# Kernel tuning notes

Hardware: AMD Instinct MI355X
Metric: run time of the kernel (lower is better)

The kernel has to match this reference:

```python
import jax, jax.numpy as jnp
import numpy as np

N_NODES = 30000
N_EDGES = 960000
HIDDEN = 256
HEADS = 4
S = 15  # num_samples
K_DIFF = 4
ALPHA = 0.1
BETA = 0.9
EPS_BN = 1e-5


def _mlp(x, W, b, g, bt, a):
    # Linear -> BatchNorm (eval: running_mean=0, running_var=1) -> PReLU
    h = x @ W + b
    h = g * h / jnp.sqrt(jnp.asarray(1.0 + EPS_BN, h.dtype)) + bt
    return jnp.where(h >= 0, h, a * h)


def _mgdcf(x, src, dst, n, k, alpha, beta):
    # Markov graph diffusion: h_k = alpha*x + beta * A_hat h_{k-1}, A_hat = D^-1/2 A D^-1/2
    ones = jnp.ones(src.shape[0], dtype=x.dtype)
    deg = jnp.maximum(jax.ops.segment_sum(ones, dst, num_segments=n), 1.0)
    norm = jax.lax.rsqrt(deg[src] * deg[dst])  # [E]
    h = x
    for _ in range(k):
        msg = jax.ops.segment_sum(h[src] * norm[:, None], dst, num_segments=n)
        h = alpha * x + beta * msg
    z = alpha * (1.0 - beta ** k) / (1.0 - beta) + beta ** k  # scale normalizer
    return h / z


def _mha(mem, Wq, bq, Wk, bk, Wv, bv, Wo, bo):
    # small-window multi-head self-attention with residual, no LN/FF
    n, s, hdim = mem.shape
    hd = hdim // HEADS
    q = (mem @ Wq + bq).reshape(n, s, HEADS, hd)
    k = (mem @ Wk + bk).reshape(n, s, HEADS, hd)
    v = (mem @ Wv + bv).reshape(n, s, HEADS, hd)
    scores = jnp.einsum('nqhd,nkhd->nhqk', q, k) / np.float32(np.sqrt(hd))
    attn = jax.nn.softmax(scores, axis=-1)
    out = jnp.einsum('nhqk,nkhd->nqhd', attn, v).reshape(n, s, hdim)
    return out @ Wo + bo + mem


def setup_inputs() -> dict:
    key = jax.random.key(0)
    ks = jax.random.split(key, 16)
    d = {}
    d['text_feat'] = jax.random.normal(ks[0], (N_NODES, 768), jnp.float32)
    d['visual_feat'] = jax.random.normal(ks[1], (N_NODES, 512), jnp.float32)
    d['edge_index'] = jax.random.randint(ks[2], (2, N_EDGES), 0, N_NODES, jnp.int32)
    d['memory_index'] = jax.random.randint(ks[3], (N_NODES, S), 0, N_NODES, jnp.int32)
    d['t_W'] = jax.random.normal(ks[4], (768, HIDDEN), jnp.float32) * np.float32(768 ** -0.5)
    d['t_b'] = jnp.zeros((HIDDEN,), jnp.float32)
    d['t_gamma'] = jnp.ones((HIDDEN,), jnp.float32)
    d['t_beta'] = jnp.zeros((HIDDEN,), jnp.float32)
    d['t_a'] = jnp.asarray(0.25, jnp.float32)
    d['v_W'] = jax.random.normal(ks[5], (512, HIDDEN), jnp.float32) * np.float32(512 ** -0.5)
    d['v_b'] = jnp.zeros((HIDDEN,), jnp.float32)
    d['v_gamma'] = jnp.ones((HIDDEN,), jnp.float32)
    d['v_beta'] = jnp.zeros((HIDDEN,), jnp.float32)
    d['v_a'] = jnp.asarray(0.25, jnp.float32)
    sc = np.float32(HIDDEN ** -0.5)
    d['Wq'] = jax.random.normal(ks[6], (HIDDEN, HIDDEN), jnp.float32) * sc
    d['bq'] = jnp.zeros((HIDDEN,), jnp.float32)
    d['Wk'] = jax.random.normal(ks[7], (HIDDEN, HIDDEN), jnp.float32) * sc
    d['bk'] = jnp.zeros((HIDDEN,), jnp.float32)
    d['Wv'] = jax.random.normal(ks[8], (HIDDEN, HIDDEN), jnp.float32) * sc
    d['bv'] = jnp.zeros((HIDDEN,), jnp.float32)
    d['Wo'] = jax.random.normal(ks[9], (HIDDEN, HIDDEN), jnp.float32) * sc
    d['bo'] = jnp.zeros((HIDDEN,), jnp.float32)
    d['Wc'] = jax.random.normal(ks[10], (HIDDEN, 40), jnp.float32) * sc
    d['bc'] = jnp.zeros((40,), jnp.float32)
    return d


def reference(text_feat, visual_feat, edge_index, memory_index,
              t_W, t_b, t_gamma, t_beta, t_a,
              v_W, v_b, v_gamma, v_beta, v_a,
              Wq, bq, Wk, bk, Wv, bv, Wo, bo, Wc, bc):
    n = text_feat.shape[0]
    src, dst = edge_index[0], edge_index[1]
    enc_t = _mlp(text_feat, t_W, t_b, t_gamma, t_beta, t_a)
    enc_v = _mlp(visual_feat, v_W, v_b, v_gamma, v_beta, v_a)
    t_h = _mgdcf(enc_t, src, dst, n, K_DIFF, ALPHA, BETA)
    v_h = _mgdcf(enc_v, src, dst, n, K_DIFF, ALPHA, BETA)
    combined = t_h + v_h  # [N, H]
    # random-memory gather: [N, S+1, H]
    mem = jnp.concatenate([combined[:, None, :], combined[memory_index]], axis=1)
    z_memory_h = _mha(mem, Wq, bq, Wk, bk, Wv, bv, Wo, bo)
    final_h = z_memory_h[:, 0]
    logits = final_h @ Wc + bc
    return logits, final_h, z_memory_h
```

## Files before the change

kernel.cpp:

```cpp
#include <hip/hip_runtime.h>
#include <math.h>

#define NN 30000
#define NE 960000
#define HID 256
#define NH 4
#define HD 64

typedef __attribute__((ext_vector_type(8))) __bf16 bf16x8;
typedef __attribute__((ext_vector_type(4))) float f32x4;
typedef __attribute__((ext_vector_type(4))) unsigned int u32x4;
typedef __attribute__((ext_vector_type(4))) unsigned short u16x4;

__device__ __forceinline__ unsigned short f2bf(float f) {
    unsigned u = __builtin_bit_cast(unsigned, f);
    u += 0x7fffu + ((u >> 16) & 1u);
    return (unsigned short)(u >> 16);
}
__device__ __forceinline__ float bf2f(unsigned short h) {
    unsigned u = ((unsigned)h) << 16;
    return __builtin_bit_cast(float, u);
}

__global__ void wsplit_k(const float* __restrict__ W, int K, int N,
                         unsigned short* __restrict__ Wh,
                         unsigned short* __restrict__ Wl)
{
    const int gid = blockIdx.x * 256 + threadIdx.x;
    if (gid >= K * N) return;
    const int k = gid / N, n = gid - k * N;
    const float f = W[gid];
    const unsigned short h = f2bf(f);
    const float lo = f - bf2f(h);
    Wh[(size_t)n * K + k] = h;
    Wl[(size_t)n * K + k] = f2bf(lo);
}

#define TBM 128
#define TBN 128
#define TBK 32
#define LDK 40

__global__ void __launch_bounds__(256) gemm_mfma(
    const float* __restrict__ A,
    const unsigned short* __restrict__ Wth,
    const unsigned short* __restrict__ Wtl,
    const float* __restrict__ bias,
    const float* __restrict__ gamma, const float* __restrict__ beta2,
    const float* __restrict__ a_ptr,
    float* __restrict__ C, int M, int N, int K, int mode)
{
    __shared__ unsigned short Ah[TBM * LDK];
    __shared__ unsigned short Al[TBM * LDK];
    __shared__ unsigned short Bh[TBN * LDK];
    __shared__ unsigned short Bl[TBN * LDK];

    const int t = threadIdx.x;
    const int bm = blockIdx.y * TBM;
    const int bn = blockIdx.x * TBN;
    const int wid = t >> 6, lane = t & 63;
    const int wm = (wid >> 1) * 64;
    const int wn = (wid & 1) * 64;
    const int fr = lane & 15;
    const int kg = lane >> 4;

    const int arow = t >> 3;
    const int ak   = (t & 7) * 4;

    f32x4 acc[4][4] = {};

    for (int k0 = 0; k0 < K; k0 += TBK) {
#pragma unroll
        for (int r = 0; r < 4; r++) {
            const int row = r * 32 + arow;
            const int gr = bm + row;
            float4 av = make_float4(0.f, 0.f, 0.f, 0.f);
            if (gr < M) av = *(const float4*)(A + (size_t)gr * K + k0 + ak);
            const unsigned short h0 = f2bf(av.x), h1 = f2bf(av.y),
                                 h2 = f2bf(av.z), h3 = f2bf(av.w);
            const unsigned short l0 = f2bf(av.x - bf2f(h0)),
                                 l1 = f2bf(av.y - bf2f(h1)),
                                 l2 = f2bf(av.z - bf2f(h2)),
                                 l3 = f2bf(av.w - bf2f(h3));
            u16x4 hv; hv.x = h0; hv.y = h1; hv.z = h2; hv.w = h3;
            u16x4 lv; lv.x = l0; lv.y = l1; lv.z = l2; lv.w = l3;
            *(u16x4*)&Ah[row * LDK + ak] = hv;
            *(u16x4*)&Al[row * LDK + ak] = lv;
        }
#pragma unroll
        for (int i2 = 0; i2 < 2; i2++) {
            const int i = i2 * 256 + t;
            const int n = i >> 2, kc = (i & 3) * 8;
            const size_t g = (size_t)(bn + n) * K + k0 + kc;
            *(u32x4*)&Bh[n * LDK + kc] = *(const u32x4*)&Wth[g];
            *(u32x4*)&Bl[n * LDK + kc] = *(const u32x4*)&Wtl[g];
        }
        __syncthreads();

        bf16x8 fah[4], fal[4], fbh[4], fbl[4];
#pragma unroll
        for (int mf = 0; mf < 4; mf++) {
            const int off = (wm + mf * 16 + fr) * LDK + kg * 8;
            fah[mf] = *(const bf16x8*)&Ah[off];
            fal[mf] = *(const bf16x8*)&Al[off];
        }
#pragma unroll
        for (int nf = 0; nf < 4; nf++) {
            const int off = (wn + nf * 16 + fr) * LDK + kg * 8;
            fbh[nf] = *(const bf16x8*)&Bh[off];
            fbl[nf] = *(const bf16x8*)&Bl[off];
        }
#pragma unroll
        for (int mf = 0; mf < 4; mf++) {
#pragma unroll
            for (int nf = 0; nf < 4; nf++) {
                acc[mf][nf] = __builtin_amdgcn_mfma_f32_16x16x32_bf16(
                    fah[mf], fbh[nf], acc[mf][nf], 0, 0, 0);
                acc[mf][nf] = __builtin_amdgcn_mfma_f32_16x16x32_bf16(
                    fah[mf], fbl[nf], acc[mf][nf], 0, 0, 0);
                acc[mf][nf] = __builtin_amdgcn_mfma_f32_16x16x32_bf16(
                    fal[mf], fbh[nf], acc[mf][nf], 0, 0, 0);
            }
        }
        __syncthreads();
    }

    const float invs = 1.0f / sqrtf(1.0f + 1e-5f);
    const float av_ = (mode != 0) ? *a_ptr : 0.f;
#pragma unroll
    for (int nf = 0; nf < 4; nf++) {
        const int c = bn + wn + nf * 16 + fr;
        const float bi = bias[c];
        float gm = 0.f, bt = 0.f;
        if (mode != 0) { gm = gamma[c]; bt = beta2[c]; }
#pragma unroll
        for (int mf = 0; mf < 4; mf++) {
#pragma unroll
            for (int i = 0; i < 4; i++) {
                const int r = bm + wm + mf * 16 + kg * 4 + i;
                if (r < M) {
                    float h = acc[mf][nf][i] + bi;
                    if (mode != 0) {
                        h = gm * h * invs + bt;
                        h = (h >= 0.f) ? h : av_ * h;
                    }
                    float* cp = C + (size_t)r * N + c;
                    if (mode == 2) h += *cp;
                    *cp = h;
                }
            }
        }
    }
}

__global__ void count_k(const int* __restrict__ dst, int* __restrict__ counts)
{
    const int e = blockIdx.x * 256 + threadIdx.x;
    if (e < NE) atomicAdd(&counts[dst[e]], 1);
}

__global__ void deg_k(const int* __restrict__ counts, float* __restrict__ deg)
{
    const int i = blockIdx.x * 256 + threadIdx.x;
    if (i < NN) deg[i] = fmaxf((float)counts[i], 1.0f);
}

__global__ void __launch_bounds__(1024) scan_k(const int* __restrict__ counts,
                                               int* __restrict__ offs, int n)
{
    __shared__ int buf[1024];
    __shared__ int carry;
    const int t = threadIdx.x;
    if (t == 0) { carry = 0; offs[0] = 0; }
    __syncthreads();
    for (int base = 0; base < n; base += 1024) {
        const int i = base + t;
        int v = (i < n) ? counts[i] : 0;
        buf[t] = v;
        __syncthreads();
        for (int off = 1; off < 1024; off <<= 1) {
            int add = (t >= off) ? buf[t - off] : 0;
            __syncthreads();
            buf[t] += add;
            __syncthreads();
        }
        if (i < n) offs[i + 1] = carry + buf[t];
        __syncthreads();
        if (t == 0) carry += buf[1023];
        __syncthreads();
    }
}

__global__ void fill_k(const int* __restrict__ src, const int* __restrict__ dst,
                       const int* __restrict__ offs, int* __restrict__ cursor,
                       const float* __restrict__ deg,
                       int* __restrict__ csrc, float* __restrict__ cw)
{
    const int e = blockIdx.x * 256 + threadIdx.x;
    if (e < NE) {
        const int d = dst[e];
        const int s = src[e];
        const int p = atomicAdd(&cursor[d], 1);
        const int slot = offs[d] + p;
        csrc[slot] = s;
        cw[slot] = rsqrtf(deg[s] * deg[d]);
    }
}

__global__ void __launch_bounds__(256) spmv_k(
    const float* __restrict__ hin, const float* __restrict__ x,
    const int* __restrict__ offs, const int* __restrict__ csrc,
    const float* __restrict__ cw, float* __restrict__ hout, float scale)
{
    const int node = blockIdx.x;
    const int t = threadIdx.x;
    const int g = t >> 6;
    const int lane = t & 63;
    const int start = offs[node], end = offs[node + 1];
    __shared__ int   ss[256];
    __shared__ float sw[256];
    __shared__ float part[4][256];
    float4 acc = make_float4(0.f, 0.f, 0.f, 0.f);
    for (int base = start; base < end; base += 256) {
        const int cnt = min(256, end - base);
        __syncthreads();
        if (t < cnt) { ss[t] = csrc[base + t]; sw[t] = cw[base + t]; }
        __syncthreads();
        for (int j = g; j < cnt; j += 4) {
            const float w = sw[j];
            const float4 v = *(const float4*)(hin + (size_t)ss[j] * HID + lane * 4);
            acc.x += v.x * w; acc.y += v.y * w;
            acc.z += v.z * w; acc.w += v.w * w;
        }
    }
    *(float4*)&part[g][lane * 4] = acc;
    __syncthreads();
    const float s = part[0][t] + part[1][t] + part[2][t] + part[3][t];
    const size_t o = (size_t)node * HID + t;
    hout[o] = (0.1f * x[o] + 0.9f * s) * scale;
}

__global__ void build_wvo(const float* __restrict__ Wv, const float* __restrict__ Wo,
                          const float* __restrict__ bv,
                          float* __restrict__ Wvo, float* __restrict__ bvo)
{
    const int gid = blockIdx.x * 256 + threadIdx.x;
    if (gid < 256 * 1024) {
        const int k = gid >> 10;
        const int col = gid & 1023;
        const int h = col >> 8, j = col & 255;
        float s = 0.f;
#pragma unroll 8
        for (int d = 0; d < HD; d++)
            s += Wv[k * HID + h * HD + d] * Wo[(h * HD + d) * HID + j];
        Wvo[(size_t)k * 1024 + col] = s;
    } else if (gid < 256 * 1024 + 1024) {
        const int col = gid - 256 * 1024;
        const int h = col >> 8, j = col & 255;
        float s = 0.f;
#pragma unroll 8
        for (int d = 0; d < HD; d++)
            s += bv[h * HD + d] * Wo[(h * HD + d) * HID + j];
        bvo[col] = s;
    }
}

__global__ void __launch_bounds__(256) attn_k(
    const float* __restrict__ Cq, const float* __restrict__ Ck,
    const float* __restrict__ P, const float* __restrict__ comb,
    const int* __restrict__ midx, const float* __restrict__ bo,
    const float* __restrict__ Wc, const float* __restrict__ bc,
    float* __restrict__ zout, float* __restrict__ fhout, float* __restrict__ lout)
{
    __shared__ float qs[16][260];
    __shared__ float ks[16][260];
    __shared__ float at2[16][NH][16];
    __shared__ float row0[256];
    __shared__ int   idx[16];
    const int n = blockIdx.x;
    const int t = threadIdx.x;

    if (t < 16) idx[t] = (t == 0) ? n : midx[n * 15 + t - 1];
    __syncthreads();
    int idr[16];
#pragma unroll
    for (int r = 0; r < 16; r++) idr[r] = idx[r];
#pragma unroll
    for (int r = 0; r < 16; r++) {
        const size_t g = (size_t)idr[r] * HID + t;
        qs[r][t] = Cq[g];
        ks[r][t] = Ck[g];
    }

    float pv[16][4];
#pragma unroll
    for (int k2 = 0; k2 < 16; k2++) {
        const float* pb = P + (size_t)idr[k2] * 1024 + t;
        pv[k2][0] = pb[0];
        pv[k2][1] = pb[256];
        pv[k2][2] = pb[512];
        pv[k2][3] = pb[768];
    }
    float cmb[16];
#pragma unroll
    for (int q2 = 0; q2 < 16; q2++)
        cmb[q2] = comb[(size_t)idr[q2] * HID + t];
    const float bov = bo[t];

    __syncthreads();

    const int kr = t & 15, qr = t >> 4;
#pragma unroll
    for (int h = 0; h < NH; h++) {
        float s = 0.f;
#pragma unroll
        for (int i = 0; i < HD; i++)
            s += qs[qr][h * HD + i] * ks[kr][h * HD + i];
        s *= 0.125f;
        float m = s;
        m = fmaxf(m, __shfl_xor(m, 1));
        m = fmaxf(m, __shfl_xor(m, 2));
        m = fmaxf(m, __shfl_xor(m, 4));
        m = fmaxf(m, __shfl_xor(m, 8));
        const float e = __expf(s - m);
        float sum = e;
        sum += __shfl_xor(sum, 1);
        sum += __shfl_xor(sum, 2);
        sum += __shfl_xor(sum, 4);
        sum += __shfl_xor(sum, 8);
        at2[qr][h][kr] = e / sum;
    }
    __syncthreads();

    float acc[16];
#pragma unroll
    for (int q2 = 0; q2 < 16; q2++) acc[q2] = cmb[q2] + bov;

#pragma unroll
    for (int q2 = 0; q2 < 16; q2++) {
        float s = acc[q2];
#pragma unroll
        for (int h = 0; h < NH; h++) {
            const f32x4* ap = (const f32x4*)&at2[q2][h][0];
            const f32x4 a0 = ap[0], a1 = ap[1], a2 = ap[2], a3 = ap[3];
            s += a0.x * pv[0][h]  + a0.y * pv[1][h]  + a0.z * pv[2][h]  + a0.w * pv[3][h]
               + a1.x * pv[4][h]  + a1.y * pv[5][h]  + a1.z * pv[6][h]  + a1.w * pv[7][h]
               + a2.x * pv[8][h]  + a2.y * pv[9][h]  + a2.z * pv[10][h] + a2.w * pv[11][h]
               + a3.x * pv[12][h] + a3.y * pv[13][h] + a3.z * pv[14][h] + a3.w * pv[15][h];
        }
        acc[q2] = s;
    }

#pragma unroll
    for (int q2 = 0; q2 < 16; q2++)
        zout[((size_t)n * 16 + q2) * HID + t] = acc[q2];
    row0[t] = acc[0];
    fhout[(size_t)n * HID + t] = acc[0];
    __syncthreads();
    if (t < 40) {
        float s = bc[t];
#pragma unroll 8
        for (int c = 0; c < 256; c++) s += row0[c] * Wc[c * 40 + t];
        lout[(size_t)n * 40 + t] = s;
    }
}

extern "C" void kernel_launch(void* const* d_in, const int* in_sizes, int n_in,
                              void* d_out, int out_size, void* d_ws, size_t ws_size,
                              hipStream_t stream)
{
    const float* text = (const float*)d_in[0];
    const float* vis  = (const float*)d_in[1];
    const int*   eidx = (const int*)d_in[2];
    const int*   midx = (const int*)d_in[3];
    const float* tW = (const float*)d_in[4];
    const float* tb = (const float*)d_in[5];
    const float* tg = (const float*)d_in[6];
    const float* tbe = (const float*)d_in[7];
    const float* ta = (const float*)d_in[8];
    const float* vW = (const float*)d_in[9];
    const float* vb = (const float*)d_in[10];
    const float* vg = (const float*)d_in[11];
    const float* vbe = (const float*)d_in[12];
    const float* va = (const float*)d_in[13];
    const float* Wq = (const float*)d_in[14];
    const float* bq = (const float*)d_in[15];
    const float* Wk = (const float*)d_in[16];
    const float* bk = (const float*)d_in[17];
    const float* Wv = (const float*)d_in[18];
    const float* bv = (const float*)d_in[19];
    const float* Wo = (const float*)d_in[20];
    const float* bo = (const float*)d_in[21];
    const float* Wc = (const float*)d_in[22];
    const float* bc = (const float*)d_in[23];

    float* out_logits = (float*)d_out;
    float* out_fh = out_logits + (size_t)NN * 40;
    float* out_z  = out_fh + (size_t)NN * HID;

    const size_t SLOT = (size_t)NN * HID;
    float* s_x   = (float*)d_ws;
    float* s_h1  = s_x + SLOT;
    float* s_h2  = s_h1 + SLOT;
    float* s_cq  = s_h2 + SLOT;
    float* s_ck  = s_cq + SLOT;
    float* s_P   = s_ck + SLOT;
    float* s_wvo = s_P + (size_t)NN * 1024;
    float* s_bvo = s_wvo + 256 * 1024;
    float* c_deg = s_bvo + 1024;
    int* c_counts = (int*)(c_deg + NN);
    int* c_off    = c_counts + NN;
    int* c_cursor = c_off + (NN + 1);
    int* c_src    = c_cursor + NN;
    float* c_w    = (float*)(c_src + NE);

    const int* e_src = eidx;
    const int* e_dst = eidx + NE;

    hipMemsetAsync(c_counts, 0, NN * sizeof(int), stream);
    hipMemsetAsync(c_cursor, 0, NN * sizeof(int), stream);

    unsigned short* tWh = (unsigned short*)s_h1;
    unsigned short* tWl = tWh + 768 * 256;
    unsigned short* vWh = tWl + 768 * 256;
    unsigned short* vWl = vWh + 512 * 256;
    wsplit_k<<<768, 256, 0, stream>>>(tW, 768, 256, tWh, tWl);
    wsplit_k<<<512, 256, 0, stream>>>(vW, 512, 256, vWh, vWl);

    const dim3 gE(HID / TBN, (NN + TBM - 1) / TBM);

    gemm_mfma<<<gE, 256, 0, stream>>>(text, tWh, tWl, tb, tg, tbe, ta, s_x, NN, HID, 768, 1);
    gemm_mfma<<<gE, 256, 0, stream>>>(vis,  vWh, vWl, vb, vg, vbe, va, s_x, NN, HID, 512, 2);

    count_k<<<NE / 256, 256, 0, stream>>>(e_dst, c_counts);
    deg_k<<<(NN + 255) / 256, 256, 0, stream>>>(c_counts, c_deg);
    scan_k<<<1, 1024, 0, stream>>>(c_counts, c_off, NN);
    fill_k<<<NE / 256, 256, 0, stream>>>(e_src, e_dst, c_off, c_cursor, c_deg, c_src, c_w);

    const double beta_k = 0.9 * 0.9 * 0.9 * 0.9;
    const double zd = 0.1 * (1.0 - beta_k) / (1.0 - 0.9) + beta_k;
    const float invz = (float)(1.0 / zd);
    spmv_k<<<NN, 256, 0, stream>>>(s_x,  s_x, c_off, c_src, c_w, s_h1, 1.0f);
    spmv_k<<<NN, 256, 0, stream>>>(s_h1, s_x, c_off, c_src, c_w, s_h2, 1.0f);
    spmv_k<<<NN, 256, 0, stream>>>(s_h2, s_x, c_off, c_src, c_w, s_h1, 1.0f);
    spmv_k<<<NN, 256, 0, stream>>>(s_h1, s_x, c_off, c_src, c_w, s_h2, invz);

    unsigned short* qWh = (unsigned short*)s_h1;
    unsigned short* qWl = qWh + 256 * 256;
    unsigned short* kWh = qWl + 256 * 256;
    unsigned short* kWl = kWh + 256 * 256;
    unsigned short* pWh = kWl + 256 * 256;
    unsigned short* pWl = pWh + 256 * 1024;
    wsplit_k<<<256, 256, 0, stream>>>(Wq, 256, 256, qWh, qWl);
    wsplit_k<<<256, 256, 0, stream>>>(Wk, 256, 256, kWh, kWl);
    build_wvo<<<(256 * 1024 + 1024) / 256, 256, 0, stream>>>(Wv, Wo, bv, s_wvo, s_bvo);
    wsplit_k<<<1024, 256, 0, stream>>>(s_wvo, 256, 1024, pWh, pWl);

    gemm_mfma<<<gE, 256, 0, stream>>>(s_h2, qWh, qWl, bq, nullptr, nullptr, nullptr, s_cq, NN, HID, HID, 0);
    gemm_mfma<<<gE, 256, 0, stream>>>(s_h2, kWh, kWl, bk, nullptr, nullptr, nullptr, s_ck, NN, HID, HID, 0);
    const dim3 gP(1024 / TBN, (NN + TBM - 1) / TBM);
    gemm_mfma<<<gP, 256, 0, stream>>>(s_h2, pWh, pWl, s_bvo, nullptr, nullptr, nullptr, s_P, NN, 1024, HID, 0);

    attn_k<<<NN, 256, 0, stream>>>(s_cq, s_ck, s_P, s_h2, midx, bo, Wc, bc,
                                   out_z, out_fh, out_logits);
}
```

Baseline: 2.275 ms.

## Compute attention scores with split-bf16 MFMA and stream z_memory stores

The scalar 64-wide dot products for the 16x16 per-head attention scores are replaced by MFMA 16x16x32 bf16 instructions, one wave per head. Q and K are stored in shared memory as high and low bf16 halves, and three MFMAs (hh, hl, lh) give close to fp32 accuracy. The change also adds a launch_bounds occupancy hint of 2 and writes the large zout tensor with nontemporal stores to avoid cache pollution. The costs are extra conversion ALU work and a small loss of precision compared with full fp32.

```diff
diff --git a/kernel.cpp b/kernel.cpp
--- a/kernel.cpp
+++ b/kernel.cpp
@@ -265,15 +265,17 @@
     }
 }
 
-__global__ void __launch_bounds__(256) attn_k(
+__global__ void __launch_bounds__(256, 2) attn_k(
     const float* __restrict__ Cq, const float* __restrict__ Ck,
     const float* __restrict__ P, const float* __restrict__ comb,
     const int* __restrict__ midx, const float* __restrict__ bo,
     const float* __restrict__ Wc, const float* __restrict__ bc,
     float* __restrict__ zout, float* __restrict__ fhout, float* __restrict__ lout)
 {
-    __shared__ float qs[16][260];
-    __shared__ float ks[16][260];
+    __shared__ unsigned short Qh[16][264];
+    __shared__ unsigned short Ql[16][264];
+    __shared__ unsigned short Kh[16][264];
+    __shared__ unsigned short Kl[16][264];
     __shared__ float at2[16][NH][16];
     __shared__ float row0[256];
     __shared__ int   idx[16];
@@ -285,12 +287,6 @@
     int idr[16];
 #pragma unroll
     for (int r = 0; r < 16; r++) idr[r] = idx[r];
-#pragma unroll
-    for (int r = 0; r < 16; r++) {
-        const size_t g = (size_t)idr[r] * HID + t;
-        qs[r][t] = Cq[g];
-        ks[r][t] = Ck[g];
-    }
 
     float pv[16][4];
 #pragma unroll
@@ -307,28 +303,50 @@
         cmb[q2] = comb[(size_t)idr[q2] * HID + t];
     const float bov = bo[t];
 
-    __syncthreads();
-
-    const int kr = t & 15, qr = t >> 4;
-#pragma unroll
-    for (int h = 0; h < NH; h++) {
-        float s = 0.f;
-#pragma unroll
-        for (int i = 0; i < HD; i++)
-            s += qs[qr][h * HD + i] * ks[kr][h * HD + i];
-        s *= 0.125f;
+#pragma unroll
+    for (int r = 0; r < 16; r++) {
+        const size_t g = (size_t)idr[r] * HID + t;
+        const float q = Cq[g];
+        const float k = Ck[g];
+        const unsigned short qh = f2bf(q);
+        const unsigned short kh = f2bf(k);
+        Qh[r][t] = qh; Ql[r][t] = f2bf(q - bf2f(qh));
+        Kh[r][t] = kh; Kl[r][t] = f2bf(k - bf2f(kh));
+    }
+    __syncthreads();
+
+    const int w  = t >> 6;
+    const int lw = t & 63;
+    const int fr = lw & 15;
+    const int kg = lw >> 4;
+
+    f32x4 sc = {};
+#pragma unroll
+    for (int ks = 0; ks < 2; ks++) {
+        const int off = w * 64 + ks * 32 + kg * 8;
+        const bf16x8 fqh = *(const bf16x8*)&Qh[fr][off];
+        const bf16x8 fql = *(const bf16x8*)&Ql[fr][off];
+        const bf16x8 fkh = *(const bf16x8*)&Kh[fr][off];
+        const bf16x8 fkl = *(const bf16x8*)&Kl[fr][off];
+        sc = __builtin_amdgcn_mfma_f32_16x16x32_bf16(fqh, fkh, sc, 0, 0, 0);
+        sc = __builtin_amdgcn_mfma_f32_16x16x32_bf16(fqh, fkl, sc, 0, 0, 0);
+        sc = __builtin_amdgcn_mfma_f32_16x16x32_bf16(fql, fkh, sc, 0, 0, 0);
+    }
+#pragma unroll
+    for (int i = 0; i < 4; i++) {
+        const float s = sc[i] * 0.125f;
         float m = s;
         m = fmaxf(m, __shfl_xor(m, 1));
         m = fmaxf(m, __shfl_xor(m, 2));
         m = fmaxf(m, __shfl_xor(m, 4));
         m = fmaxf(m, __shfl_xor(m, 8));
         const float e = __expf(s - m);
-        float sum = e;
-        sum += __shfl_xor(sum, 1);
-        sum += __shfl_xor(sum, 2);
-        sum += __shfl_xor(sum, 4);
-        sum += __shfl_xor(sum, 8);
-        at2[qr][h][kr] = e / sum;
+        float su = e;
+        su += __shfl_xor(su, 1);
+        su += __shfl_xor(su, 2);
+        su += __shfl_xor(su, 4);
+        su += __shfl_xor(su, 8);
+        at2[kg * 4 + i][w][fr] = e / su;
     }
     __syncthreads();
 
@@ -353,7 +371,7 @@
 
 #pragma unroll
     for (int q2 = 0; q2 < 16; q2++)
-        zout[((size_t)n * 16 + q2) * HID + t] = acc[q2];
+        __builtin_nontemporal_store(acc[q2], &zout[((size_t)n * 16 + q2) * HID + t]);
     row0[t] = acc[0];
     fhout[(size_t)n * HID + t] = acc[0];
     __syncthreads();
```

Measured after the change: 2.287 ms. Within noise of the previous version (+0.5%).
